# Kernel optimization log

Measured on AMD Instinct MI355X. Metric: run time of the kernel, lower is better.

Reference implementation:

```python
import jax, jax.numpy as jnp
import numpy as np

B, S, D, H = 4, 2048, 1024, 16
DH = D // H
LN_EPS = 1e-5


def setup_inputs() -> dict:
    key = jax.random.key(0)
    ks = jax.random.split(key, 12)
    scale = 0.02
    inp = {
        "x": jax.random.normal(ks[0], (B, S, D), dtype=jnp.float32),
        "attention_mask": jnp.ones((B, 1, 1, S), dtype=jnp.int32),
        # Linear weights stored torch-style: (out_features, in_features)
        "Wq": jax.random.normal(ks[1], (D, D), dtype=jnp.float32) * scale,
        "bq": jax.random.normal(ks[2], (D,), dtype=jnp.float32) * scale,
        "Wk": jax.random.normal(ks[3], (D, D), dtype=jnp.float32) * scale,
        "bk": jax.random.normal(ks[4], (D,), dtype=jnp.float32) * scale,
        "Wv": jax.random.normal(ks[5], (D, D), dtype=jnp.float32) * scale,
        "bv": jax.random.normal(ks[6], (D,), dtype=jnp.float32) * scale,
        "Wo": jax.random.normal(ks[7], (D, D), dtype=jnp.float32) * scale,
        "bo": jax.random.normal(ks[8], (D,), dtype=jnp.float32) * scale,
        "ln_w": jnp.ones((D,), dtype=jnp.float32),
        "ln_b": jnp.zeros((D,), dtype=jnp.float32),
    }
    return inp


def reference(x, attention_mask, Wq, bq, Wk, bk, Wv, bv, Wo, bo, ln_w, ln_b):
    b, s, d = x.shape
    # QKV projections (torch Linear: x @ W.T + b), split into heads -> [b, h, s, dh]
    def proj(W, bias):
        y = jnp.einsum('bsd,ed->bse', x, W) + bias
        return y.reshape(b, s, H, DH).transpose(0, 2, 1, 3)
    q = proj(Wq, bq)
    k = proj(Wk, bk)
    v = proj(Wv, bv)

    scores = jnp.einsum('bhqd,bhkd->bhqk', q, k) / jnp.sqrt(jnp.float32(DH))
    scores = jnp.where(attention_mask == 0, -jnp.inf, scores)
    # max-subtract softmax (stable), identical to jax.nn.softmax
    attn = jax.nn.softmax(scores, axis=-1)
    Hctx = jnp.einsum('bhqk,bhkd->bhqd', attn, v)  # [b, h, s, dh]
    Hctx = Hctx.transpose(0, 2, 1, 3).reshape(b, s, d)

    Hout = jnp.einsum('bsd,ed->bse', Hctx, Wo) + bo
    resid = x + Hout
    mu = jnp.mean(resid, axis=-1, keepdims=True)
    var = jnp.mean(jnp.square(resid - mu), axis=-1, keepdims=True)
    out = (resid - mu) / jnp.sqrt(var + LN_EPS) * ln_w + ln_b
    return out
```

## Files before the change

kernel.cpp:

```cpp
#include <hip/hip_runtime.h>
#include <hip/hip_bf16.h>
#include <stdint.h>

#define Bx  4
#define Sx  2048
#define Dx  1024
#define Hx  16
#define DHx 64
#define Mx  (Bx*Sx)

typedef short bf16x8 __attribute__((ext_vector_type(8)));
typedef float f32x4  __attribute__((ext_vector_type(4)));
typedef float f32x16 __attribute__((ext_vector_type(16)));

#define C1 0.18033688f

__device__ __forceinline__ unsigned short f2bf_u(float f) {
  union { float f; unsigned int u; } c; c.f = f;
  return (unsigned short)((c.u + 0x7fffu + ((c.u >> 16) & 1u)) >> 16);
}
__device__ __forceinline__ unsigned int pack2(float lo, float hi) {
  return ((unsigned int)f2bf_u(hi) << 16) | (unsigned int)f2bf_u(lo);
}
__device__ __forceinline__ unsigned int cvtpk(float lo_, float hi_) {
  unsigned int r;
  asm("v_cvt_pk_bf16_f32 %0, %1, %2" : "=v"(r) : "v"(lo_), "v"(hi_));
  return r;
}
__device__ __forceinline__ void swap32(unsigned int& d, unsigned int& s) {
  asm("v_permlane32_swap_b32 %0, %1" : "+v"(d), "+v"(s));
}

#define GLDS16(gp, lp) __builtin_amdgcn_global_load_lds( \
  (const __attribute__((address_space(1))) unsigned int*)(gp), \
  (__attribute__((address_space(3))) unsigned int*)(lp), 16, 0, 0)

__global__ __launch_bounds__(256) void prep_kernel(
    const float* __restrict__ x,  const float* __restrict__ Wq,
    const float* __restrict__ Wk, const float* __restrict__ Wv,
    const float* __restrict__ Wo, const int* __restrict__ mask,
    uint4* __restrict__ xb4, uint4* __restrict__ wb4,
    float* __restrict__ madd, unsigned* __restrict__ mb) {
  int bid = blockIdx.x, t = threadIdx.x;
  if (bid < 6144) {
    const float* src;
    uint4* dst;
    int i;
    if (bid < 4096) {
      src = x; dst = xb4; i = bid * 256 + t;
    } else {
      int wbid = bid - 4096;
      int widx = wbid >> 9;
      src = (widx == 0) ? Wq : (widx == 1) ? Wk : (widx == 2) ? Wv : Wo;
      dst = wb4 + (size_t)widx * 131072;
      i = (wbid & 511) * 256 + t;
    }
    const float4* s = (const float4*)src + (size_t)i * 2;
    float4 a = s[0], b = s[1];
    uint4 o;
    o.x = pack2(a.x, a.y); o.y = pack2(a.z, a.w);
    o.z = pack2(b.x, b.y); o.w = pack2(b.z, b.w);
    int ip = (i & ~3) | ((i & 3) ^ ((i >> 7) & 3) ^ ((i >> 9) & 3));
    dst[ip] = o;
  } else if (bid < 6176) {
    int i = (bid - 6144) * 256 + t;
    madd[i] = (mask[i] == 0) ? -1e30f : 0.0f;
  } else {
    int b = bid - 6176;
    if (t < 64) {
      int any = 0;
      if (t < 32) {
        for (int i = 0; i < 64; ++i) any |= (mask[b * Sx + t * 64 + i] == 0);
      }
      unsigned long long bits = __ballot(any != 0);
      if (t == 0) mb[b] = (unsigned)bits;
    }
  }
}

__global__ __launch_bounds__(256) void qkv_gemm(
    const short* __restrict__ xb, const short* __restrict__ wb,
    const float* __restrict__ bq, const float* __restrict__ bk,
    const float* __restrict__ bv,
    short* __restrict__ qb, short* __restrict__ kb, short* __restrict__ vb) {
  int lid = blockIdx.x + (blockIdx.y << 3) + (blockIdx.z << 9);
  int xcd = lid & 7;
  int idx = lid >> 3;
  int which = idx >> 6;
  int tt = idx & 63;
  int m0 = (xcd * 8 + (tt >> 3)) * 128;
  int n0 = (tt & 7) * 128;

  const short* Wm  = wb + (size_t)which * Dx * Dx;
  const float* bias = (which == 0) ? bq : (which == 1 ? bk : bv);

  __shared__ alignas(16) short smem[128 * 136];

  int t = threadIdx.x;
  int l = t & 63, w = t >> 6;
  int wm = w >> 1, wn = w & 1;
  int srow = l >> 2;
  int scol = (l & 3) * 8;
  int fr = l & 15, fg = l >> 4;
  int pl = (fr & 3) ^ ((fr >> 2) & 3);
  int cA = ((fg ^ pl) << 3);

  int r0a = (w * 2 + 0) * 16;
  int r0b = (w * 2 + 1) * 16;
  const short* gA0 = xb + (size_t)(m0 + r0a + srow) * Dx + scol;
  const short* gA1 = xb + (size_t)(m0 + r0b + srow) * Dx + scol;
  const short* gB0 = Wm + (size_t)(n0 + r0a + srow) * Dx + scol;
  const short* gB1 = Wm + (size_t)(n0 + r0b + srow) * Dx + scol;

  f32x4 acc[4][4] = {};

#define QSTAGE(step, bf) do {                                             \
    size_t ko = (size_t)(step) * 32;                                      \
    GLDS16(gA0 + ko, &smem[(bf) * 8192 + r0a * 32]);                      \
    GLDS16(gB0 + ko, &smem[(bf) * 8192 + 4096 + r0a * 32]);               \
    GLDS16(gA1 + ko, &smem[(bf) * 8192 + r0b * 32]);                      \
    GLDS16(gB1 + ko, &smem[(bf) * 8192 + 4096 + r0b * 32]);               \
  } while (0)

#define QBODY(step, cur) do {                                             \
    if ((step) < 31) {                                                    \
      QSTAGE((step) + 1, (cur) ^ 1);                                      \
      asm volatile("s_waitcnt vmcnt(4)" ::: "memory");                    \
    } else {                                                              \
      asm volatile("s_waitcnt vmcnt(0)" ::: "memory");                    \
    }                                                                     \
    __builtin_amdgcn_s_barrier();                                         \
    const short* Al = &smem[(cur) * 8192];                                \
    const short* Bl = &smem[(cur) * 8192 + 4096];                         \
    bf16x8 af[4], bfm[4];                                                 \
    _Pragma("unroll")                                                     \
    for (int i = 0; i < 4; ++i)                                           \
      af[i] = *(const bf16x8*)&Al[(wm * 64 + i * 16 + fr) * 32 + cA];     \
    _Pragma("unroll")                                                     \
    for (int i = 0; i < 4; ++i)                                           \
      bfm[i] = *(const bf16x8*)&Bl[(wn * 64 + i * 16 + fr) * 32 + cA];    \
    _Pragma("unroll")                                                     \
    for (int mi = 0; mi < 4; ++mi)                                        \
      _Pragma("unroll")                                                   \
      for (int ni = 0; ni < 4; ++ni)                                      \
        acc[mi][ni] = __builtin_amdgcn_mfma_f32_16x16x32_bf16(            \
            af[mi], bfm[ni], acc[mi][ni], 0, 0, 0);                       \
    __builtin_amdgcn_s_barrier();                                         \
  } while (0)

  QSTAGE(0, 0);

  for (int ks = 0; ks < 32; ks += 2) {
    QBODY(ks, 0);
    QBODY(ks + 1, 1);
  }
#undef QBODY
#undef QSTAGE

  if (which == 2) {
    __syncthreads();
#pragma unroll
    for (int ni = 0; ni < 4; ++ni) {
      int n_l = wn * 64 + ni * 16 + fr;
      float bias_n = bias[n0 + n_l];
#pragma unroll
      for (int mi = 0; mi < 4; ++mi)
#pragma unroll
        for (int r = 0; r < 4; ++r) {
          int m_l = wm * 64 + mi * 16 + fg * 4 + r;
          smem[n_l * 136 + m_l] = (short)f2bf_u(acc[mi][ni][r] + bias_n);
        }
    }
    __syncthreads();
    int b = m0 >> 11, s0_ = m0 & 2047;
#pragma unroll
    for (int it = 0; it < 8; ++it) {
      int idx2 = t + it * 256;
      int n_l = idx2 >> 4, c = idx2 & 15;
      int4 v = *(const int4*)&smem[n_l * 136 + c * 8];
      int n = n0 + n_l, h = n >> 6, dh = n & 63;
      int chunk = (c & 7) ^ (dh & 7);
      size_t off = (size_t)(b * Hx + h) * Sx * 64
                 + (size_t)((s0_ >> 6) + (c >> 3)) * 4096
                 + dh * 64 + chunk * 8;
      *(int4*)&vb[off] = v;
    }
    return;
  }

#pragma unroll
  for (int ni = 0; ni < 4; ++ni) {
    int n = n0 + wn * 64 + ni * 16 + fr;
    int h = n >> 6, dh = n & 63;
    float bias_n = bias[n];
#pragma unroll
    for (int mi = 0; mi < 4; ++mi) {
#pragma unroll
      for (int r = 0; r < 4; ++r) {
        int m = m0 + wm * 64 + mi * 16 + fg * 4 + r;
        int b = m >> 11, s = m & 2047;
        float y = acc[mi][ni][r] + bias_n;
        size_t hb = (size_t)(b * Hx + h) * Sx * DHx;
        if (which == 0) {
          qb[hb + (size_t)s * DHx + dh] = (short)f2bf_u(y * C1);
        } else {
          kb[hb + (size_t)s * 64 + ((((dh >> 3) ^ (s & 7)) << 3) | (dh & 7))] =
              (short)f2bf_u(y);
        }
      }
    }
  }
}

__global__ __launch_bounds__(256, 2) void attn_kernel(
    const short* __restrict__ qb, const short* __restrict__ kb,
    const short* __restrict__ vb, const float* __restrict__ madd,
    const unsigned* __restrict__ maskbits, short* __restrict__ cbuf) {
  int bh = blockIdx.x;
  int qt = blockIdx.y;
  int b  = bh >> 4;

  __shared__ alignas(16) short Kl[2][4096];
  __shared__ alignas(16) short Vt[2][4096];

  int t = threadIdx.x, l = t & 63, w = t >> 6;
  int lo = l & 31, hi = l >> 5;

  const short* qgA = qb + ((size_t)bh * Sx + qt * 256 + w * 64 + lo) * 64;
  const short* qgB = qgA + 32 * 64;
  bf16x8 qfA[4], qfB[4];
#pragma unroll
  for (int ks = 0; ks < 4; ++ks) {
    qfA[ks] = *(const bf16x8*)&qgA[ks * 16 + hi * 8];
    qfB[ks] = *(const bf16x8*)&qgB[ks * 16 + hi * 8];
  }

  int koff[4], koff32[4];
#pragma unroll
  for (int ks = 0; ks < 4; ++ks) {
    int c = ((2 * ks + hi) ^ (lo & 7)) << 3;
    koff[ks]   = lo * 64 + c;
    koff32[ks] = (32 + lo) * 64 + c;
  }

  const short* kg = kb + (size_t)bh * Sx * 64;
  const short* vg = vb + (size_t)bh * Sx * 64;
  const float* mg = madd + b * Sx;
  unsigned mbits = maskbits[b];

  bf16x8 ones;
#pragma unroll
  for (int i = 0; i < 8; ++i) ones[i] = (short)0x3F80;

  f32x16 OA0 = {}, OA1 = {}, SsA = {};
  f32x16 OB0 = {}, OB1 = {}, SsB = {};

#define STAGE(tile, bf) do {                                              \
    const short* ks_ = kg + (size_t)(tile) * 4096;                        \
    const short* vs_ = vg + (size_t)(tile) * 4096;                        \
    GLDS16(ks_ + w * 512 + l * 8,        &Kl[bf][w * 512]);               \
    GLDS16(ks_ + 2048 + w * 512 + l * 8, &Kl[bf][2048 + w * 512]);        \
    GLDS16(vs_ + w * 512 + l * 8,        &Vt[bf][w * 512]);               \
    GLDS16(vs_ + 2048 + w * 512 + l * 8, &Vt[bf][2048 + w * 512]);        \
  } while (0)

#define TBODY(tile, cur) do {                                             \
    if ((tile) < 31) {                                                    \
      STAGE((tile) + 1, (cur) ^ 1);                                       \
      asm volatile("s_waitcnt vmcnt(4)" ::: "memory");                    \
    } else {                                                              \
      asm volatile("s_waitcnt vmcnt(0)" ::: "memory");                    \
    }                                                                     \
    __builtin_amdgcn_s_barrier();                                         \
    const short* Kb = &Kl[cur][0];                                        \
    const short* Vb = &Vt[cur][0];                                        \
    f32x16 sA0 = {}, sA1 = {}, sB0 = {}, sB1 = {};                        \
    __builtin_amdgcn_s_setprio(1);                                        \
    _Pragma("unroll")                                                     \
    for (int ks = 0; ks < 4; ++ks) {                                      \
      bf16x8 kf = *(const bf16x8*)&Kb[koff[ks]];                          \
      sA0 = __builtin_amdgcn_mfma_f32_32x32x16_bf16(kf, qfA[ks], sA0, 0, 0, 0); \
      sB0 = __builtin_amdgcn_mfma_f32_32x32x16_bf16(kf, qfB[ks], sB0, 0, 0, 0); \
    }                                                                     \
    _Pragma("unroll")                                                     \
    for (int ks = 0; ks < 4; ++ks) {                                      \
      bf16x8 kf = *(const bf16x8*)&Kb[koff32[ks]];                        \
      sA1 = __builtin_amdgcn_mfma_f32_32x32x16_bf16(kf, qfA[ks], sA1, 0, 0, 0); \
      sB1 = __builtin_amdgcn_mfma_f32_32x32x16_bf16(kf, qfB[ks], sB1, 0, 0, 0); \
    }                                                                     \
    __builtin_amdgcn_s_setprio(0);                                        \
    if ((mbits >> (tile)) & 1) {                                          \
      const float* mrow = mg + (tile) * 64;                               \
      _Pragma("unroll")                                                   \
      for (int r = 0; r < 16; ++r) {                                      \
        int key = (r & 3) + 8 * (r >> 2) + 4 * hi;                        \
        float m0_ = mrow[key], m1_ = mrow[32 + key];                      \
        sA0[r] += m0_; sA1[r] += m1_;                                     \
        sB0[r] += m0_; sB1[r] += m1_;                                     \
      }                                                                   \
    }                                                                     \
    _Pragma("unroll")                                                     \
    for (int r = 0; r < 16; ++r) {                                        \
      sA0[r] = __builtin_amdgcn_exp2f(sA0[r]);                            \
      sA1[r] = __builtin_amdgcn_exp2f(sA1[r]);                            \
      sB0[r] = __builtin_amdgcn_exp2f(sB0[r]);                            \
      sB1[r] = __builtin_amdgcn_exp2f(sB1[r]);                            \
    }                                                                     \
    __builtin_amdgcn_s_setprio(1);                                        \
    _Pragma("unroll")                                                     \
    for (int kbi = 0; kbi < 2; ++kbi) {                                   \
      _Pragma("unroll")                                                   \
      for (int half = 0; half < 2; ++half) {                              \
        int po = half * 8;                                                \
        unsigned int uA, uA2, vA, vA2, uB, uB2, vB, vB2;                  \
        if (kbi == 0) {                                                   \
          uA  = cvtpk(sA0[po + 0], sA0[po + 1]);                          \
          uA2 = cvtpk(sA0[po + 2], sA0[po + 3]);                          \
          vA  = cvtpk(sA0[po + 4], sA0[po + 5]);                          \
          vA2 = cvtpk(sA0[po + 6], sA0[po + 7]);                          \
          uB  = cvtpk(sB0[po + 0], sB0[po + 1]);                          \
          uB2 = cvtpk(sB0[po + 2], sB0[po + 3]);                          \
          vB  = cvtpk(sB0[po + 4], sB0[po + 5]);                          \
          vB2 = cvtpk(sB0[po + 6], sB0[po + 7]);                          \
        } else {                                                          \
          uA  = cvtpk(sA1[po + 0], sA1[po + 1]);                          \
          uA2 = cvtpk(sA1[po + 2], sA1[po + 3]);                          \
          vA  = cvtpk(sA1[po + 4], sA1[po + 5]);                          \
          vA2 = cvtpk(sA1[po + 6], sA1[po + 7]);                          \
          uB  = cvtpk(sB1[po + 0], sB1[po + 1]);                          \
          uB2 = cvtpk(sB1[po + 2], sB1[po + 3]);                          \
          vB  = cvtpk(sB1[po + 4], sB1[po + 5]);                          \
          vB2 = cvtpk(sB1[po + 6], sB1[po + 7]);                          \
        }                                                                 \
        swap32(vA, uA); swap32(vA2, uA2);                                 \
        swap32(vB, uB); swap32(vB2, uB2);                                 \
        union { unsigned int i[4]; bf16x8 v8; } puA, puB;                 \
        puA.i[0] = uA; puA.i[1] = uA2; puA.i[2] = vA; puA.i[3] = vA2;     \
        puB.i[0] = uB; puB.i[1] = uB2; puB.i[2] = vB; puB.i[3] = vB2;     \
        int vi = kbi * 2 + half;                                          \
        bf16x8 vf0 = *(const bf16x8*)&Vb[koff[vi]];                       \
        bf16x8 vf1 = *(const bf16x8*)&Vb[koff32[vi]];                     \
        OA0 = __builtin_amdgcn_mfma_f32_32x32x16_bf16(puA.v8, vf0, OA0, 0, 0, 0); \
        OA1 = __builtin_amdgcn_mfma_f32_32x32x16_bf16(puA.v8, vf1, OA1, 0, 0, 0); \
        SsA = __builtin_amdgcn_mfma_f32_32x32x16_bf16(puA.v8, ones, SsA, 0, 0, 0); \
        OB0 = __builtin_amdgcn_mfma_f32_32x32x16_bf16(puB.v8, vf0, OB0, 0, 0, 0); \
        OB1 = __builtin_amdgcn_mfma_f32_32x32x16_bf16(puB.v8, vf1, OB1, 0, 0, 0); \
        SsB = __builtin_amdgcn_mfma_f32_32x32x16_bf16(puB.v8, ones, SsB, 0, 0, 0); \
      }                                                                   \
    }                                                                     \
    __builtin_amdgcn_s_setprio(0);                                        \
    __builtin_amdgcn_s_barrier();                                        \
  } while (0)

  STAGE(0, 0);

  for (int tile = 0; tile < 32; tile += 2) {
    TBODY(tile, 0);
    TBODY(tile + 1, 1);
  }
#undef TBODY
#undef STAGE

  int h = bh & 15, bq_ = bh >> 4;
  int loLo = lo & 7, loCh = lo >> 3;
#pragma unroll
  for (int a = 0; a < 4; ++a) {
#pragma unroll
    for (int j = 0; j < 4; ++j) {
      int r = a * 4 + j;
      int srow = a * 8 + hi * 4 + j;
      int p = (srow & 3) ^ ((srow >> 2) & 3);
      int colp = ((loCh ^ p) << 3) | loLo;
      float linvA = __builtin_amdgcn_rcpf(SsA[r]);
      float linvB = __builtin_amdgcn_rcpf(SsB[r]);
      int sA = qt * 256 + w * 64 + srow;
      int sB = sA + 32;
      size_t rowbA = ((size_t)(bq_ * Sx + sA)) * Dx + h * 64;
      size_t rowbB = ((size_t)(bq_ * Sx + sB)) * Dx + h * 64;
      cbuf[rowbA + colp]      = (short)f2bf_u(OA0[r] * linvA);
      cbuf[rowbA + 32 + colp] = (short)f2bf_u(OA1[r] * linvA);
      cbuf[rowbB + colp]      = (short)f2bf_u(OB0[r] * linvB);
      cbuf[rowbB + 32 + colp] = (short)f2bf_u(OB1[r] * linvB);
    }
  }
}

__global__ __launch_bounds__(256) void proj_gemm(
    const short* __restrict__ cb, const short* __restrict__ wo,
    const float* __restrict__ bo, const float* __restrict__ x,
    float* __restrict__ out) {
  int lid = blockIdx.x + (blockIdx.y << 3);
  int xcd = lid & 7;
  int tt = lid >> 3;
  int m0 = (xcd * 8 + (tt >> 3)) * 128;
  int n0 = (tt & 7) * 128;

  __shared__ alignas(16) short Al[128 * 32];
  __shared__ alignas(16) short Bl[128 * 32];

  int t = threadIdx.x;
  int l = t & 63, w = t >> 6;
  int wm = w >> 1, wn = w & 1;
  int srow = l >> 2, scol = (l & 3) * 8;
  int fr = l & 15, fg = l >> 4;
  int pl = (fr & 3) ^ ((fr >> 2) & 3);
  int cA = ((fg ^ pl) << 3);

  f32x4 acc[4][4] = {};

  for (int k0 = 0; k0 < Dx; k0 += 32) {
#pragma unroll
    for (int i = 0; i < 2; ++i) {
      int r0 = (w * 2 + i) * 16;
      const short* ga = cb + (size_t)(m0 + r0 + srow) * Dx + k0 + scol;
      GLDS16(ga, &Al[r0 * 32]);
      const short* gb = wo + (size_t)(n0 + r0 + srow) * Dx + k0 + scol;
      GLDS16(gb, &Bl[r0 * 32]);
    }
    __syncthreads();
    bf16x8 af[4], bfm[4];
#pragma unroll
    for (int i = 0; i < 4; ++i)
      af[i] = *(const bf16x8*)&Al[(wm * 64 + i * 16 + fr) * 32 + cA];
#pragma unroll
    for (int i = 0; i < 4; ++i)
      bfm[i] = *(const bf16x8*)&Bl[(wn * 64 + i * 16 + fr) * 32 + cA];
#pragma unroll
    for (int mi = 0; mi < 4; ++mi)
#pragma unroll
      for (int ni = 0; ni < 4; ++ni)
        acc[mi][ni] = __builtin_amdgcn_mfma_f32_16x16x32_bf16(
            af[mi], bfm[ni], acc[mi][ni], 0, 0, 0);
    __syncthreads();
  }

#pragma unroll
  for (int ni = 0; ni < 4; ++ni) {
    int n = n0 + wn * 64 + ni * 16 + fr;
    float bias_n = bo[n];
#pragma unroll
    for (int mi = 0; mi < 4; ++mi) {
#pragma unroll
      for (int r = 0; r < 4; ++r) {
        int m = m0 + wm * 64 + mi * 16 + fg * 4 + r;
        float y = acc[mi][ni][r] + bias_n + x[(size_t)m * Dx + n];
        out[(size_t)m * Dx + n] = y;
      }
    }
  }
}

__global__ __launch_bounds__(256) void ln_kernel(float* __restrict__ io,
                                                 const float* __restrict__ lw,
                                                 const float* __restrict__ lb) {
  int row = blockIdx.x;
  float* p = io + (size_t)row * Dx;
  int c = threadIdx.x * 4;
  float4 v = *(float4*)&p[c];
  float s = v.x + v.y + v.z + v.w;
  float q = v.x * v.x + v.y * v.y + v.z * v.z + v.w * v.w;
#pragma unroll
  for (int d = 1; d < 64; d <<= 1) {
    s += __shfl_xor(s, d, 64);
    q += __shfl_xor(q, d, 64);
  }
  __shared__ float ss[4], qq[4];
  int l = threadIdx.x & 63, w = threadIdx.x >> 6;
  if (l == 0) { ss[w] = s; qq[w] = q; }
  __syncthreads();
  s = ss[0] + ss[1] + ss[2] + ss[3];
  q = qq[0] + qq[1] + qq[2] + qq[3];
  float mu = s * (1.f / Dx);
  float var = q * (1.f / Dx) - mu * mu;
  float rstd = rsqrtf(var + 1e-5f);
  float4 w4 = *(const float4*)&lw[c];
  float4 b4 = *(const float4*)&lb[c];
  float4 o;
  o.x = (v.x - mu) * rstd * w4.x + b4.x;
  o.y = (v.y - mu) * rstd * w4.y + b4.y;
  o.z = (v.z - mu) * rstd * w4.z + b4.z;
  o.w = (v.w - mu) * rstd * w4.w + b4.w;
  *(float4*)&p[c] = o;
}

extern "C" void kernel_launch(void* const* d_in, const int* in_sizes, int n_in,
                              void* d_out, int out_size, void* d_ws, size_t ws_size,
                              hipStream_t stream) {
  const float* x   = (const float*)d_in[0];
  const int*   msk = (const int*)d_in[1];
  const float* Wq  = (const float*)d_in[2];
  const float* bq  = (const float*)d_in[3];
  const float* Wk  = (const float*)d_in[4];
  const float* bk  = (const float*)d_in[5];
  const float* Wv  = (const float*)d_in[6];
  const float* bv  = (const float*)d_in[7];
  const float* Wo  = (const float*)d_in[8];
  const float* bo  = (const float*)d_in[9];
  const float* lnw = (const float*)d_in[10];
  const float* lnb = (const float*)d_in[11];
  float* out = (float*)d_out;

  char* ws = (char*)d_ws;
  short* xb = (short*)(ws);
  short* wb = (short*)(ws + (size_t)(16 << 20));
  short* qb = (short*)(ws + (size_t)(24 << 20));
  short* kb = (short*)(ws + (size_t)(40 << 20));
  short* vb = (short*)(ws + (size_t)(56 << 20));
  short* cb = (short*)(ws + (size_t)(72 << 20));
  float* madd = out;
  unsigned* mbits = (unsigned*)(out + Mx);

  prep_kernel<<<6180, 256, 0, stream>>>(x, Wq, Wk, Wv, Wo, msk,
                                        (uint4*)xb, (uint4*)wb, madd, mbits);
  qkv_gemm<<<dim3(8, 64, 3), 256, 0, stream>>>(xb, wb, bq, bk, bv, qb, kb, vb);
  attn_kernel<<<dim3(64, 8), 256, 0, stream>>>(qb, kb, vb, madd, mbits, cb);
  proj_gemm<<<dim3(8, 64), 256, 0, stream>>>(cb, wb + 3 * (size_t)(Dx * Dx), bo, x, out);
  ln_kernel<<<Mx, 256, 0, stream>>>(out, lnw, lnb);
}
```

Measured before the change: 202.1 us.

## Double-buffer LDS staging in output projection GEMM to overlap loads

The output-projection GEMM now uses two LDS buffers and issues the global-to-LDS loads for the next K step before computing on the current one, waiting with a partial vmcnt. It also hoists the per-row global pointers out of the loop. The aim is to hide global load latency behind MFMA work instead of stalling on a full sync each K step. The cost is doubled LDS use, which may reduce occupancy.

```diff
diff --git a/kernel.cpp b/kernel.cpp
--- a/kernel.cpp
+++ b/kernel.cpp
@@ -266,7 +266,7 @@
 
 #define TBODY(tile, cur) do {                                             \
     if ((tile) < 31) {                                                    \
-      STAGE((tile) + 1, (cur) ^ 1);                                       \
+      STAGE((tile) + 1, (cur) ^ 1);                                      \
       asm volatile("s_waitcnt vmcnt(4)" ::: "memory");                    \
     } else {                                                              \
       asm volatile("s_waitcnt vmcnt(0)" ::: "memory");                    \
@@ -395,8 +395,7 @@
   int m0 = (xcd * 8 + (tt >> 3)) * 128;
   int n0 = (tt & 7) * 128;
 
-  __shared__ alignas(16) short Al[128 * 32];
-  __shared__ alignas(16) short Bl[128 * 32];
+  __shared__ alignas(16) short smem[2 * 8192];
 
   int t = threadIdx.x;
   int l = t & 63, w = t >> 6;
@@ -406,33 +405,57 @@
   int pl = (fr & 3) ^ ((fr >> 2) & 3);
   int cA = ((fg ^ pl) << 3);
 
+  int r0a = (w * 2 + 0) * 16;
+  int r0b = (w * 2 + 1) * 16;
+  const short* gA0 = cb + (size_t)(m0 + r0a + srow) * Dx + scol;
+  const short* gA1 = cb + (size_t)(m0 + r0b + srow) * Dx + scol;
+  const short* gB0 = wo + (size_t)(n0 + r0a + srow) * Dx + scol;
+  const short* gB1 = wo + (size_t)(n0 + r0b + srow) * Dx + scol;
+
   f32x4 acc[4][4] = {};
 
-  for (int k0 = 0; k0 < Dx; k0 += 32) {
-#pragma unroll
-    for (int i = 0; i < 2; ++i) {
-      int r0 = (w * 2 + i) * 16;
-      const short* ga = cb + (size_t)(m0 + r0 + srow) * Dx + k0 + scol;
-      GLDS16(ga, &Al[r0 * 32]);
-      const short* gb = wo + (size_t)(n0 + r0 + srow) * Dx + k0 + scol;
-      GLDS16(gb, &Bl[r0 * 32]);
-    }
-    __syncthreads();
-    bf16x8 af[4], bfm[4];
-#pragma unroll
-    for (int i = 0; i < 4; ++i)
-      af[i] = *(const bf16x8*)&Al[(wm * 64 + i * 16 + fr) * 32 + cA];
-#pragma unroll
-    for (int i = 0; i < 4; ++i)
-      bfm[i] = *(const bf16x8*)&Bl[(wn * 64 + i * 16 + fr) * 32 + cA];
-#pragma unroll
-    for (int mi = 0; mi < 4; ++mi)
-#pragma unroll
-      for (int ni = 0; ni < 4; ++ni)
-        acc[mi][ni] = __builtin_amdgcn_mfma_f32_16x16x32_bf16(
-            af[mi], bfm[ni], acc[mi][ni], 0, 0, 0);
-    __syncthreads();
-  }
+#define PSTAGE(step, bf) do {                                             \
+    size_t ko = (size_t)(step) * 32;                                      \
+    GLDS16(gA0 + ko, &smem[(bf) * 8192 + r0a * 32]);                      \
+    GLDS16(gB0 + ko, &smem[(bf) * 8192 + 4096 + r0a * 32]);               \
+    GLDS16(gA1 + ko, &smem[(bf) * 8192 + r0b * 32]);                      \
+    GLDS16(gB1 + ko, &smem[(bf) * 8192 + 4096 + r0b * 32]);               \
+  } while (0)
+
+#define PBODY(step, cur) do {                                             \
+    if ((step) < 31) {                                                    \
+      PSTAGE((step) + 1, (cur) ^ 1);                                      \
+      asm volatile("s_waitcnt vmcnt(4)" ::: "memory");                    \
+    } else {                                                              \
+      asm volatile("s_waitcnt vmcnt(0)" ::: "memory");                    \
+    }                                                                     \
+    __builtin_amdgcn_s_barrier();                                         \
+    const short* Al = &smem[(cur) * 8192];                                \
+    const short* Bl = &smem[(cur) * 8192 + 4096];                         \
+    bf16x8 af[4], bfm[4];                                                 \
+    _Pragma("unroll")                                                     \
+    for (int i = 0; i < 4; ++i)                                           \
+      af[i] = *(const bf16x8*)&Al[(wm * 64 + i * 16 + fr) * 32 + cA];     \
+    _Pragma("unroll")                                                     \
+    for (int i = 0; i < 4; ++i)                                           \
+      bfm[i] = *(const bf16x8*)&Bl[(wn * 64 + i * 16 + fr) * 32 + cA];    \
+    _Pragma("unroll")                                                     \
+    for (int mi = 0; mi < 4; ++mi)                                        \
+      _Pragma("unroll")                                                   \
+      for (int ni = 0; ni < 4; ++ni)                                      \
+        acc[mi][ni] = __builtin_amdgcn_mfma_f32_16x16x32_bf16(            \
+            af[mi], bfm[ni], acc[mi][ni], 0, 0, 0);                       \
+    __builtin_amdgcn_s_barrier();                                         \
+  } while (0)
+
+  PSTAGE(0, 0);
+
+  for (int ks = 0; ks < 32; ks += 2) {
+    PBODY(ks, 0);
+    PBODY(ks + 1, 1);
+  }
+#undef PBODY
+#undef PSTAGE
 
 #pragma unroll
   for (int ni = 0; ni < 4; ++ni) {
```

New measurement: 201.7 us. No clear change (-0.2%).
